# Kernel optimization log

Hardware: AMD Instinct MI355X
Metric: run time of the kernel (lower is better)

## Reference

```python
import jax, jax.numpy as jnp
import numpy as np

B, I, O, G = 262144, 3, 64, 128


def setup_inputs() -> dict:
    key = jax.random.key(0)
    kx, kc = jax.random.split(key)
    x = jax.random.uniform(kx, (1, B, I), dtype=jnp.float32)  # coords in [0,1)
    coeffs = jax.random.normal(kc, (2, O, I, G), dtype=jnp.float32) / (
        np.float32(np.sqrt(I) * np.sqrt(G))
    )
    bias = jnp.zeros((1, O), dtype=jnp.float32)
    return {"x": x, "coeffs": coeffs, "bias": bias}


def reference(x, coeffs, bias):
    # x: (1, B, I); coeffs: (2, O, I, G); bias: (1, O)
    b, i = x.shape[1], x.shape[2]
    two, o, _, g = coeffs.shape
    k = jnp.arange(1, g + 1, dtype=x.dtype)          # (G,)
    kx = x.reshape(b, i, 1) * k                      # (B, I, G)
    cosf = jnp.cos(kx).reshape(b, i * g)             # (B, I*G)
    sinf = jnp.sin(kx).reshape(b, i * g)             # (B, I*G)
    w = coeffs.reshape(2, o, i * g)                  # (2, O, I*G)
    # sum over (input_dim, gridsize) fused as one GEMM per trig branch
    out = cosf @ w[0].T + sinf @ w[1].T + bias       # (B, O)
    return out
```

## Files before the change

### kernel.cpp

```cpp
#include <hip/hip_runtime.h>
#include <hip/hip_fp16.h>

typedef __attribute__((ext_vector_type(8))) short short8;
typedef __attribute__((ext_vector_type(8))) _Float16 half8;
typedef __attribute__((ext_vector_type(4))) float f32x4;
typedef __attribute__((ext_vector_type(2))) float f32x2;
typedef __attribute__((ext_vector_type(4))) unsigned int u32x4;

#define NROWS   262144
#define ODIM    64
#define NBLOCKS 256
#define TPB     1024
#define INV2PI  0.15915494309189535f

__device__ __forceinline__ float cos2pi(float f){ float r; asm("v_cos_f32 %0, %1" : "=v"(r) : "v"(f)); return r; }
__device__ __forceinline__ float sin2pi(float f){ float r; asm("v_sin_f32 %0, %1" : "=v"(r) : "v"(f)); return r; }

__device__ __forceinline__ short f16_of(float f){
    union { _Float16 h; short s; } u; u.h = (_Float16)f; return u.s; }
__device__ __forceinline__ unsigned h2b(__half2 h){
    union { __half2 h; unsigned u; } x; x.h = h; return x.u; }
__device__ __forceinline__ half8 u4h(u32x4 v){ union{u32x4 u; half8 h;} x; x.u = v; return x.h; }
__device__ __forceinline__ half8 s8h(short8 v){ union{short8 s; half8 h;} x; x.s = v; return x.h; }

#define ADV(C, S, RC, RS, RN) do {                       \
    const __half2 _cn = __hfma2(C, RC, __hmul2(S, RN));  \
    const __half2 _sn = __hfma2(S, RC, __hmul2(C, RS));  \
    C = _cn; S = _sn;                                    \
} while (0)

extern "C" __global__ void __launch_bounds__(TPB, 4)
__attribute__((amdgpu_waves_per_eu(4, 4)))
fourier_mfma(const float* __restrict__ x,
             const float* __restrict__ coeffs,
             const float* __restrict__ bias,
             float* __restrict__ out)
{
    __shared__ short8 Wlds[24 * 4 * 64];

    const int tid = threadIdx.x;

    for (int fl = tid; fl < 24*4*64; fl += TPB) {
        const int ks = fl >> 8;
        const int nt = (fl >> 6) & 3;
        const int ln = fl & 63;
        const int o  = nt*16 + (ln & 15);
        const int kg = ln >> 4;
        union { short8 v; short s[8]; } fr;
        #pragma unroll
        for (int h = 0; h < 2; ++h) {
            const int kb  = ks*32 + h*16;
            const int br  = (kb >= 384) ? 1 : 0;
            const int rem = kb - br*384;
            const int ii  = rem >> 7;
            const int g0  = (rem & 127) + kg*4;
            const float* wp = coeffs + (((br*ODIM + o)*3 + ii) << 7) + g0;
            #pragma unroll
            for (int j = 0; j < 4; ++j) fr.s[h*4 + j] = f16_of(wp[j]);
        }
        Wlds[fl] = fr.v;
    }
    __syncthreads();

    const int lane = tid & 63;
    const int wid  = tid >> 6;
    const int mrow = lane & 15;
    const int kgrp = lane >> 4;
    const float hs = (float)(4*kgrp + 1);

    float bcol[4];
    #pragma unroll
    for (int nt = 0; nt < 4; ++nt) bcol[nt] = bias[nt*16 + mrow];

    const int unit = blockIdx.x * 16 + wid;
    const int base = unit * 64;

    #pragma unroll 1
    for (int rg = 0; rg < 2; ++rg) {
        const int rowA = base + (rg*2 + 0)*16 + mrow;
        const int rowB = base + (rg*2 + 1)*16 + mrow;

        f32x2 xr[3];
        #pragma unroll
        for (int i = 0; i < 3; ++i)
            xr[i] = (f32x2){ x[rowA*3 + i] * INV2PI, x[rowB*3 + i] * INV2PI };

        f32x4 acc[2][4];
        #pragma unroll
        for (int rr = 0; rr < 2; ++rr)
            #pragma unroll
            for (int nt = 0; nt < 4; ++nt)
                acc[rr][nt] = (f32x4){0.f, 0.f, 0.f, 0.f};

        __half2 C0, S0, C1, S1;
        __half2 c2h0, s2h0, n2h0, c14h0, s14h0, n14h0;
        __half2 c2h1, s2h1, n2h1, c14h1, s14h1, n14h1;

        #pragma unroll 1
        for (int kk = 0; kk < 12; ++kk) {
            short8 bfr[8];
            #pragma unroll
            for (int nt = 0; nt < 4; ++nt) {
                bfr[nt]     = Wlds[(kk*4 + nt)*64 + lane];
                bfr[4 + nt] = Wlds[((kk + 12)*4 + nt)*64 + lane];
            }

            if ((kk & 3) == 0) {
                const int i = kk >> 2;
                const f32x2 a = xr[i];
                {
                    const float av = a.x;
                    float u0 = hs*av;        u0 -= floorf(u0);
                    float u1 = (hs+1.f)*av;  u1 -= floorf(u1);
                    C0 = __floats2half2_rn(cos2pi(u0), cos2pi(u1));
                    S0 = __floats2half2_rn(sin2pi(u0), sin2pi(u1));
                    float t2 = 2.f*av;       t2 -= floorf(t2);
                    const float c2 = cos2pi(t2), s2 = sin2pi(t2);
                    float t14 = 14.f*av;     t14 -= floorf(t14);
                    const float c14 = cos2pi(t14), s14 = sin2pi(t14);
                    c2h0  = __float2half2_rn(c2);   s2h0  = __float2half2_rn(s2);
                    n2h0  = __float2half2_rn(-s2);
                    c14h0 = __float2half2_rn(c14);  s14h0 = __float2half2_rn(s14);
                    n14h0 = __float2half2_rn(-s14);
                }
                {
                    const float av = a.y;
                    float u0 = hs*av;        u0 -= floorf(u0);
                    float u1 = (hs+1.f)*av;  u1 -= floorf(u1);
                    C1 = __floats2half2_rn(cos2pi(u0), cos2pi(u1));
                    S1 = __floats2half2_rn(sin2pi(u0), sin2pi(u1));
                    float t2 = 2.f*av;       t2 -= floorf(t2);
                    const float c2 = cos2pi(t2), s2 = sin2pi(t2);
                    float t14 = 14.f*av;     t14 -= floorf(t14);
                    const float c14 = cos2pi(t14), s14 = sin2pi(t14);
                    c2h1  = __float2half2_rn(c2);   s2h1  = __float2half2_rn(s2);
                    n2h1  = __float2half2_rn(-s2);
                    c14h1 = __float2half2_rn(c14);  s14h1 = __float2half2_rn(s14);
                    n14h1 = __float2half2_rn(-s14);
                }
            }

            u32x4 FCA, FSA;
            FCA.x = h2b(C0); FSA.x = h2b(S0);
            ADV(C0, S0, c2h0,  s2h0,  n2h0);
            FCA.y = h2b(C0); FSA.y = h2b(S0);
            ADV(C0, S0, c14h0, s14h0, n14h0);
            FCA.z = h2b(C0); FSA.z = h2b(S0);
            ADV(C0, S0, c2h0,  s2h0,  n2h0);
            FCA.w = h2b(C0); FSA.w = h2b(S0);
            ADV(C0, S0, c14h0, s14h0, n14h0);
            const half8 fAc = u4h(FCA), fAs = u4h(FSA);

            #pragma unroll
            for (int nt = 0; nt < 4; ++nt)
                acc[0][nt] = __builtin_amdgcn_mfma_f32_16x16x32_f16(fAc, s8h(bfr[nt]), acc[0][nt], 0, 0, 0);

            u32x4 FCB, FSB;
            FCB.x = h2b(C1); FSB.x = h2b(S1);
            ADV(C1, S1, c2h1,  s2h1,  n2h1);
            FCB.y = h2b(C1); FSB.y = h2b(S1);
            ADV(C1, S1, c14h1, s14h1, n14h1);
            FCB.z = h2b(C1); FSB.z = h2b(S1);
            ADV(C1, S1, c2h1,  s2h1,  n2h1);
            FCB.w = h2b(C1); FSB.w = h2b(S1);
            ADV(C1, S1, c14h1, s14h1, n14h1);
            const half8 fBc = u4h(FCB), fBs = u4h(FSB);

            #pragma unroll
            for (int nt = 0; nt < 4; ++nt)
                acc[0][nt] = __builtin_amdgcn_mfma_f32_16x16x32_f16(fAs, s8h(bfr[4+nt]), acc[0][nt], 0, 0, 0);
            #pragma unroll
            for (int nt = 0; nt < 4; ++nt)
                acc[1][nt] = __builtin_amdgcn_mfma_f32_16x16x32_f16(fBc, s8h(bfr[nt]),   acc[1][nt], 0, 0, 0);
            #pragma unroll
            for (int nt = 0; nt < 4; ++nt)
                acc[1][nt] = __builtin_amdgcn_mfma_f32_16x16x32_f16(fBs, s8h(bfr[4+nt]), acc[1][nt], 0, 0, 0);
        }

        #pragma unroll
        for (int rr = 0; rr < 2; ++rr) {
            const int row0 = base + (rg*2 + rr)*16 + kgrp*4;
            #pragma unroll
            for (int nt = 0; nt < 4; ++nt) {
                #pragma unroll
                for (int q = 0; q < 4; ++q) {
                    out[(row0 + q)*ODIM + nt*16 + mrow] = acc[rr][nt][q] + bcol[nt];
                }
            }
        }
    }
}

extern "C" void kernel_launch(void* const* d_in, const int* in_sizes, int n_in,
                              void* d_out, int out_size, void* d_ws, size_t ws_size,
                              hipStream_t stream) {
    const float* x      = (const float*)d_in[0];
    const float* coeffs = (const float*)d_in[1];
    const float* bias   = (const float*)d_in[2];
    float* out = (float*)d_out;
    (void)in_sizes; (void)n_in; (void)out_size; (void)d_ws; (void)ws_size;
    hipLaunchKernelGGL(fourier_mfma, dim3(NBLOCKS), dim3(TPB), 0, stream, x, coeffs, bias, out);
}
```

Baseline: 38.89 us.

## Software-pipeline LDS weight loads and feature generation against MFMA chains

Restructures the K loop so the LDS weight fragments and the cos/sin features for the next iteration are produced while the current iteration's MFMAs run. The cosine-branch MFMAs for both row tiles are grouped first so the cosine weight registers can be refilled early, then the sine registers are refilled. The anchor and rotation walk for the next step now run at the end of each iteration. This aims to hide LDS latency and VALU trig/rotation work behind matrix ops, at the cost of more live registers under a 4-waves-per-EU bound.

```diff
diff --git a/kernel.cpp b/kernel.cpp
--- a/kernel.cpp
+++ b/kernel.cpp
@@ -27,6 +27,53 @@
     const __half2 _cn = __hfma2(C, RC, __hmul2(S, RN));  \
     const __half2 _sn = __hfma2(S, RC, __hmul2(C, RS));  \
     C = _cn; S = _sn;                                    \
+} while (0)
+
+#define WALK() do {                                       \
+    FCA.x = h2b(C0); FSA.x = h2b(S0);                     \
+    FCB.x = h2b(C1); FSB.x = h2b(S1);                     \
+    ADV(C0, S0, c2h0,  s2h0,  n2h0);  ADV(C1, S1, c2h1,  s2h1,  n2h1);  \
+    FCA.y = h2b(C0); FSA.y = h2b(S0);                     \
+    FCB.y = h2b(C1); FSB.y = h2b(S1);                     \
+    ADV(C0, S0, c14h0, s14h0, n14h0); ADV(C1, S1, c14h1, s14h1, n14h1); \
+    FCA.z = h2b(C0); FSA.z = h2b(S0);                     \
+    FCB.z = h2b(C1); FSB.z = h2b(S1);                     \
+    ADV(C0, S0, c2h0,  s2h0,  n2h0);  ADV(C1, S1, c2h1,  s2h1,  n2h1);  \
+    FCA.w = h2b(C0); FSA.w = h2b(S0);                     \
+    FCB.w = h2b(C1); FSB.w = h2b(S1);                     \
+    ADV(C0, S0, c14h0, s14h0, n14h0); ADV(C1, S1, c14h1, s14h1, n14h1); \
+} while (0)
+
+#define ANCHOR(I) do {                                    \
+    const f32x2 a = xr[I];                                \
+    {   const float av = a.x;                             \
+        float u0 = hs*av;        u0 -= floorf(u0);        \
+        float u1 = (hs+1.f)*av;  u1 -= floorf(u1);        \
+        C0 = __floats2half2_rn(cos2pi(u0), cos2pi(u1));   \
+        S0 = __floats2half2_rn(sin2pi(u0), sin2pi(u1));   \
+        float t2 = 2.f*av;       t2 -= floorf(t2);        \
+        const float c2 = cos2pi(t2), s2 = sin2pi(t2);     \
+        float t14 = 14.f*av;     t14 -= floorf(t14);      \
+        const float c14 = cos2pi(t14), s14 = sin2pi(t14); \
+        c2h0  = __float2half2_rn(c2);   s2h0  = __float2half2_rn(s2);   \
+        n2h0  = __float2half2_rn(-s2);                    \
+        c14h0 = __float2half2_rn(c14);  s14h0 = __float2half2_rn(s14);  \
+        n14h0 = __float2half2_rn(-s14);                   \
+    }                                                     \
+    {   const float av = a.y;                             \
+        float u0 = hs*av;        u0 -= floorf(u0);        \
+        float u1 = (hs+1.f)*av;  u1 -= floorf(u1);        \
+        C1 = __floats2half2_rn(cos2pi(u0), cos2pi(u1));   \
+        S1 = __floats2half2_rn(sin2pi(u0), sin2pi(u1));   \
+        float t2 = 2.f*av;       t2 -= floorf(t2);        \
+        const float c2 = cos2pi(t2), s2 = sin2pi(t2);     \
+        float t14 = 14.f*av;     t14 -= floorf(t14);      \
+        const float c14 = cos2pi(t14), s14 = sin2pi(t14); \
+        c2h1  = __float2half2_rn(c2);   s2h1  = __float2half2_rn(s2);   \
+        n2h1  = __float2half2_rn(-s2);                    \
+        c14h1 = __float2half2_rn(c14);  s14h1 = __float2half2_rn(s14);  \
+        n14h1 = __float2half2_rn(-s14);                   \
+    }                                                     \
 } while (0)
 
 extern "C" __global__ void __launch_bounds__(TPB, 4)
@@ -96,85 +143,51 @@
         __half2 c2h0, s2h0, n2h0, c14h0, s14h0, n14h0;
         __half2 c2h1, s2h1, n2h1, c14h1, s14h1, n14h1;
 
+        u32x4 FCA, FSA, FCB, FSB;
+        ANCHOR(0);
+        WALK();
+        short8 bfr[8];
+        #pragma unroll
+        for (int nt = 0; nt < 4; ++nt) {
+            bfr[nt]     = Wlds[(0*4 + nt)*64 + lane];
+            bfr[4 + nt] = Wlds[(12*4 + nt)*64 + lane];
+        }
+
         #pragma unroll 1
         for (int kk = 0; kk < 12; ++kk) {
-            short8 bfr[8];
-            #pragma unroll
-            for (int nt = 0; nt < 4; ++nt) {
-                bfr[nt]     = Wlds[(kk*4 + nt)*64 + lane];
-                bfr[4 + nt] = Wlds[((kk + 12)*4 + nt)*64 + lane];
-            }
-
-            if ((kk & 3) == 0) {
-                const int i = kk >> 2;
-                const f32x2 a = xr[i];
-                {
-                    const float av = a.x;
-                    float u0 = hs*av;        u0 -= floorf(u0);
-                    float u1 = (hs+1.f)*av;  u1 -= floorf(u1);
-                    C0 = __floats2half2_rn(cos2pi(u0), cos2pi(u1));
-                    S0 = __floats2half2_rn(sin2pi(u0), sin2pi(u1));
-                    float t2 = 2.f*av;       t2 -= floorf(t2);
-                    const float c2 = cos2pi(t2), s2 = sin2pi(t2);
-                    float t14 = 14.f*av;     t14 -= floorf(t14);
-                    const float c14 = cos2pi(t14), s14 = sin2pi(t14);
-                    c2h0  = __float2half2_rn(c2);   s2h0  = __float2half2_rn(s2);
-                    n2h0  = __float2half2_rn(-s2);
-                    c14h0 = __float2half2_rn(c14);  s14h0 = __float2half2_rn(s14);
-                    n14h0 = __float2half2_rn(-s14);
-                }
-                {
-                    const float av = a.y;
-                    float u0 = hs*av;        u0 -= floorf(u0);
-                    float u1 = (hs+1.f)*av;  u1 -= floorf(u1);
-                    C1 = __floats2half2_rn(cos2pi(u0), cos2pi(u1));
-                    S1 = __floats2half2_rn(sin2pi(u0), sin2pi(u1));
-                    float t2 = 2.f*av;       t2 -= floorf(t2);
-                    const float c2 = cos2pi(t2), s2 = sin2pi(t2);
-                    float t14 = 14.f*av;     t14 -= floorf(t14);
-                    const float c14 = cos2pi(t14), s14 = sin2pi(t14);
-                    c2h1  = __float2half2_rn(c2);   s2h1  = __float2half2_rn(s2);
-                    n2h1  = __float2half2_rn(-s2);
-                    c14h1 = __float2half2_rn(c14);  s14h1 = __float2half2_rn(s14);
-                    n14h1 = __float2half2_rn(-s14);
-                }
-            }
-
-            u32x4 FCA, FSA;
-            FCA.x = h2b(C0); FSA.x = h2b(S0);
-            ADV(C0, S0, c2h0,  s2h0,  n2h0);
-            FCA.y = h2b(C0); FSA.y = h2b(S0);
-            ADV(C0, S0, c14h0, s14h0, n14h0);
-            FCA.z = h2b(C0); FSA.z = h2b(S0);
-            ADV(C0, S0, c2h0,  s2h0,  n2h0);
-            FCA.w = h2b(C0); FSA.w = h2b(S0);
-            ADV(C0, S0, c14h0, s14h0, n14h0);
-            const half8 fAc = u4h(FCA), fAs = u4h(FSA);
+            const half8 fAc = u4h(FCA), fBc = u4h(FCB);
+            const half8 fAs = u4h(FSA), fBs = u4h(FSB);
 
             #pragma unroll
             for (int nt = 0; nt < 4; ++nt)
                 acc[0][nt] = __builtin_amdgcn_mfma_f32_16x16x32_f16(fAc, s8h(bfr[nt]), acc[0][nt], 0, 0, 0);
-
-            u32x4 FCB, FSB;
-            FCB.x = h2b(C1); FSB.x = h2b(S1);
-            ADV(C1, S1, c2h1,  s2h1,  n2h1);
-            FCB.y = h2b(C1); FSB.y = h2b(S1);
-            ADV(C1, S1, c14h1, s14h1, n14h1);
-            FCB.z = h2b(C1); FSB.z = h2b(S1);
-            ADV(C1, S1, c2h1,  s2h1,  n2h1);
-            FCB.w = h2b(C1); FSB.w = h2b(S1);
-            ADV(C1, S1, c14h1, s14h1, n14h1);
-            const half8 fBc = u4h(FCB), fBs = u4h(FSB);
+            #pragma unroll
+            for (int nt = 0; nt < 4; ++nt)
+                acc[1][nt] = __builtin_amdgcn_mfma_f32_16x16x32_f16(fBc, s8h(bfr[nt]), acc[1][nt], 0, 0, 0);
+
+            if (kk < 11) {
+                #pragma unroll
+                for (int nt = 0; nt < 4; ++nt)
+                    bfr[nt] = Wlds[((kk+1)*4 + nt)*64 + lane];
+            }
 
             #pragma unroll
             for (int nt = 0; nt < 4; ++nt)
                 acc[0][nt] = __builtin_amdgcn_mfma_f32_16x16x32_f16(fAs, s8h(bfr[4+nt]), acc[0][nt], 0, 0, 0);
             #pragma unroll
             for (int nt = 0; nt < 4; ++nt)
-                acc[1][nt] = __builtin_amdgcn_mfma_f32_16x16x32_f16(fBc, s8h(bfr[nt]),   acc[1][nt], 0, 0, 0);
-            #pragma unroll
-            for (int nt = 0; nt < 4; ++nt)
                 acc[1][nt] = __builtin_amdgcn_mfma_f32_16x16x32_f16(fBs, s8h(bfr[4+nt]), acc[1][nt], 0, 0, 0);
+
+            if (kk < 11) {
+                #pragma unroll
+                for (int nt = 0; nt < 4; ++nt)
+                    bfr[4+nt] = Wlds[((kk+13)*4 + nt)*64 + lane];
+            }
+
+            if (kk < 11) {
+                if (((kk+1) & 3) == 0) ANCHOR((kk+1) >> 2);
+                WALK();
+            }
         }
 
         #pragma unroll
```

Result: slower. 39.75 us (+2.2%).
